# Optimization experiments

Hardware: AMD Instinct MI355X
Metric: run time of the kernel (lower is better)

The kernel has to match this reference:

```python
import jax, jax.numpy as jnp
import numpy as np

N = 8192
E = 262144
EMBD = 64
NIN = 16
K = 4

def setup_inputs() -> dict:
    key = jax.random.key(0)
    k1, k2, k3, k4 = jax.random.split(key, 4)
    node_features = jax.random.normal(k1, (N, EMBD), dtype=jnp.float32)
    edge_index = jax.random.randint(k2, (2, E), 0, N, dtype=jnp.int64)
    edge_weights = jax.random.uniform(k3, (E,), dtype=jnp.float32)
    # xavier_uniform for Emb [embdsize, nin]
    limit = float(np.sqrt(6.0 / (EMBD + NIN)))
    Emb = jax.random.uniform(k4, (EMBD, NIN), dtype=jnp.float32, minval=-limit, maxval=limit)
    return {"node_features": node_features, "edge_index": edge_index,
            "edge_weights": edge_weights, "Emb": Emb}

def reference(node_features, edge_index, edge_weights, Emb):
    # embed: [N, embdsize] @ [embdsize, nin] -> [N, nin]
    x = node_features @ Emb
    # matching torch fancy-index assignment)
    A = jnp.zeros((N, N), dtype=x.dtype).at[edge_index[0], edge_index[1]].set(edge_weights)
    def step(h, _):
        h = A @ h
        return h, h
    _, data_out = jax.lax.scan(step, x, None, length=K)  # [K, N, nin]
    return data_out
```

## Files before the change

kernel.cpp:

```cpp
#include <hip/hip_runtime.h>

#define N_NODES 8192
#define E_EDGES 262144
#define EMBDSZ  64
#define NIN     16
#define K_STEPS 4
#define ROWCAP  96
#define NBLK    1024
#define NTHR    256
#define NGRP    32
#define GRPSZ   32

typedef unsigned long long u64;
typedef unsigned u32;
typedef float f32x4 __attribute__((ext_vector_type(4)));

#define AT_LOAD(p)     __hip_atomic_load((p), __ATOMIC_RELAXED, __HIP_MEMORY_SCOPE_AGENT)
#define AT_STORE(p, v) __hip_atomic_store((p), (v), __ATOMIC_RELAXED, __HIP_MEMORY_SCOPE_AGENT)
#define AT_ADD(p, v)   __hip_atomic_fetch_add((p), (v), __ATOMIC_RELAXED, __HIP_MEMORY_SCOPE_AGENT)

__device__ __forceinline__ void store_f4_sc1(float* p, f32x4 v) {
    asm volatile("global_store_dwordx4 %0, %1, off sc1" :: "v"(p), "v"(v) : "memory");
}

__global__ void init_kernel(u32* __restrict__ cursor, u32* __restrict__ bar) {
    int t = threadIdx.x;
    uint4 z = make_uint4(0, 0, 0, 0);
    #pragma unroll
    for (int i = 0; i < 8; ++i) ((uint4*)cursor)[t + i * NTHR] = z;
    #pragma unroll
    for (int i = 0; i < 2; ++i) ((uint4*)bar)[t + i * NTHR] = z;
}

__global__ void embed_scatter_kernel(const float* __restrict__ nf,
                                     const float* __restrict__ emb,
                                     const int*   __restrict__ ei,
                                     const float* __restrict__ ew,
                                     float* __restrict__ x0,
                                     u32*   __restrict__ cursor,
                                     u64*   __restrict__ rowdat) {
    __shared__ float semb[EMBDSZ * NIN];
    const int b = blockIdx.x, tid = threadIdx.x;
    for (int i = tid; i < EMBDSZ * NIN; i += NTHR) semb[i] = emb[i];
    __syncthreads();
    int gt = b * NTHR + tid;
    {
        int o = gt >> 1, half = gt & 1;
        int n = o >> 4, jj = o & 15;
        const f32x4* nfp = (const f32x4*)(nf + n * EMBDSZ + half * 32);
        const float* ep  = semb + half * 32 * NIN + jj;
        float acc = 0.f;
        #pragma unroll
        for (int k8 = 0; k8 < 8; ++k8) {
            f32x4 a = nfp[k8];
            acc += a.x * ep[(k8 * 4 + 0) * NIN] + a.y * ep[(k8 * 4 + 1) * NIN]
                 + a.z * ep[(k8 * 4 + 2) * NIN] + a.w * ep[(k8 * 4 + 3) * NIN];
        }
        acc += __shfl_xor(acc, 1);
        if (half == 0) x0[o] = acc;
    }
    {
        int e = gt;
        u32 r  = (u32)ei[e];
        u32 c  = (u32)ei[E_EDGES + e];
        u32 wb = __float_as_uint(ew[e]);
        u32 slot = atomicAdd(&cursor[r], 1u);
        if (slot < ROWCAP)
            rowdat[(size_t)r * ROWCAP + slot] =
                ((u64)wb << 32) | (u64)(c << 18) | (u64)(u32)e;
    }
}

__device__ __forceinline__ void grid_barrier(u32* bar, u32 phase) {
    asm volatile("s_waitcnt vmcnt(0)" ::: "memory");
    __syncthreads();
    if (threadIdx.x == 0) {
        u32 g = (u32)blockIdx.x >> 5;
        if (AT_ADD(&bar[g * 16], 1u) == phase * GRPSZ - 1u) {
            if (AT_ADD(&bar[512], 1u) == phase * NGRP - 1u) {
                #pragma unroll
                for (u32 gg = 0; gg < NGRP; ++gg)
                    AT_STORE(&bar[528 + gg * 16], phase);
            }
        }
        while (AT_LOAD(&bar[528 + g * 16]) < phase) __builtin_amdgcn_s_sleep(1);
    }
    __syncthreads();
}

__global__ void __launch_bounds__(NTHR, 4) spmm_persist(
    const u32*   __restrict__ cursor,
    const u64*   __restrict__ rowdat,
    const float* __restrict__ x0,
    float* __restrict__ out,
    u32*   __restrict__ bar)
{
    __shared__ u64 srow[4][2][ROWCAP];
    const int b = blockIdx.x, tid = threadIdx.x;
    const int wid = tid >> 6, lane = tid & 63;
    const int slane = lane & 15, f4 = lane >> 4;
    const int wave = b * 4 + wid;

    u32 len[2];
    #pragma unroll
    for (int rr = 0; rr < 2; ++rr) {
        int row = wave * 2 + rr;
        u32 L = min(cursor[row], (u32)ROWCAP);
        len[rr] = L;
        const u64* rp = rowdat + (size_t)row * ROWCAP;
        for (u32 i = lane; i < L; i += 64) srow[wid][rr][i] = rp[i];
    }
    #pragma unroll
    for (int rr = 0; rr < 2; ++rr) {
        u32 L = len[rr];
        for (u32 i = lane; i < L; i += 64) {
            u64 v = srow[wid][rr][i];
            u32 lo = (u32)v;
            bool dead = false;
            for (u32 q = 0; q < L; ++q) {
                u32 o = (u32)srow[wid][rr][q];
                dead |= ((o >> 18) == (lo >> 18)) && (o > lo);
            }
            if (dead) srow[wid][rr][i] = (u64)lo;
        }
    }
    const float* hin = x0;
    for (int k = 0; k < K_STEPS; ++k) {
        if (k > 0) grid_barrier(bar, (u32)k);
        float* hout = out + (size_t)k * N_NODES * NIN;
        #pragma unroll
        for (int rr = 0; rr < 2; ++rr) {
            int row = wave * 2 + rr;
            u32 L = len[rr];
            f32x4 acc = {0.f, 0.f, 0.f, 0.f};
            for (u32 i = slane; i < L; i += 16) {
                u64 v = srow[wid][rr][i];
                float w = __uint_as_float((u32)(v >> 32));
                u32 c = ((u32)v) >> 18;
                f32x4 h = *(const f32x4*)&hin[c * NIN + f4 * 4];
                acc += w * h;
            }
            #pragma unroll
            for (int d = 1; d < 16; d <<= 1) {
                acc.x += __shfl_xor(acc.x, d);
                acc.y += __shfl_xor(acc.y, d);
                acc.z += __shfl_xor(acc.z, d);
                acc.w += __shfl_xor(acc.w, d);
            }
            if (slane == 0) store_f4_sc1(&hout[row * NIN + f4 * 4], acc);
        }
        hin = hout;
    }
}

extern "C" void kernel_launch(void* const* d_in, const int* in_sizes, int n_in,
                              void* d_out, int out_size, void* d_ws, size_t ws_size,
                              hipStream_t stream) {
    (void)in_sizes; (void)n_in; (void)out_size; (void)ws_size;
    const float* nf  = (const float*)d_in[0];
    const int*   ei  = (const int*)d_in[1];
    const float* ew  = (const float*)d_in[2];
    const float* emb = (const float*)d_in[3];
    float* out = (float*)d_out;

    char* ws = (char*)d_ws;
    size_t off = 0;
    auto alloc = [&](size_t bytes) {
        void* p = ws + off;
        off += (bytes + 255) & ~(size_t)255;
        return p;
    };
    u64*   rowdat = (u64*)alloc((size_t)N_NODES * ROWCAP * 8);
    float* x0     = (float*)alloc((size_t)N_NODES * NIN * 4);
    u32*   cursor = (u32*)alloc((size_t)N_NODES * 4);
    u32*   bar    = (u32*)alloc(8192);

    init_kernel<<<1, NTHR, 0, stream>>>(cursor, bar);
    embed_scatter_kernel<<<1024, NTHR, 0, stream>>>(nf, emb, ei, ew, x0, cursor, rowdat);
    spmm_persist<<<NBLK, NTHR, 0, stream>>>(cursor, rowdat, x0, out, bar);
}
```

Before: 58.08 us.

## Fuse embed/scatter into persistent kernel and replace grid barriers with per-row progress flags

Merges the embedding/scatter kernel and the persistent SpMM kernel into one launch, separated by a single flat atomic-counter grid barrier. The per-step hierarchical grid barriers are replaced by dataflow sync: each wave publishes a per-row progress counter after writing its rows, and before each step it polls the counters of the source rows in its adjacency list. This removes one kernel launch and lets waves proceed as soon as their neighbors are ready. In exchange it adds many polled atomic loads per step and a contended single counter for the first barrier.

Result: slower. 144.8 us (+149.3%).

```diff
diff --git a/kernel.cpp b/kernel.cpp
--- a/kernel.cpp
+++ b/kernel.cpp
@@ -8,8 +8,6 @@
 #define ROWCAP  96
 #define NBLK    1024
 #define NTHR    256
-#define NGRP    32
-#define GRPSZ   32
 
 typedef unsigned long long u64;
 typedef unsigned u32;
@@ -22,28 +20,44 @@
 __device__ __forceinline__ void store_f4_sc1(float* p, f32x4 v) {
     asm volatile("global_store_dwordx4 %0, %1, off sc1" :: "v"(p), "v"(v) : "memory");
 }
-
-__global__ void init_kernel(u32* __restrict__ cursor, u32* __restrict__ bar) {
-    int t = threadIdx.x;
-    uint4 z = make_uint4(0, 0, 0, 0);
-    #pragma unroll
-    for (int i = 0; i < 8; ++i) ((uint4*)cursor)[t + i * NTHR] = z;
-    #pragma unroll
-    for (int i = 0; i < 2; ++i) ((uint4*)bar)[t + i * NTHR] = z;
+__device__ __forceinline__ void store_u64_sc1(u64* p, u64 v) {
+    asm volatile("global_store_dwordx2 %0, %1, off sc1" :: "v"(p), "v"(v) : "memory");
+}
+__device__ __forceinline__ void store_f32_sc1(float* p, float v) {
+    asm volatile("global_store_dword %0, %1, off sc1" :: "v"(p), "v"(v) : "memory");
 }
 
-__global__ void embed_scatter_kernel(const float* __restrict__ nf,
-                                     const float* __restrict__ emb,
-                                     const int*   __restrict__ ei,
-                                     const float* __restrict__ ew,
-                                     float* __restrict__ x0,
-                                     u32*   __restrict__ cursor,
-                                     u64*   __restrict__ rowdat) {
+__global__ void init_kernel(u32* __restrict__ cursor, u32* __restrict__ prog,
+                            u32* __restrict__ done) {
+    int t = blockIdx.x * NTHR + threadIdx.x;
+    cursor[t] = 0;
+    prog[t]   = 0;
+    if (t == 0) *done = 0;
+}
+
+__global__ void __launch_bounds__(NTHR, 4) mega_kernel(
+    const float* __restrict__ nf,
+    const float* __restrict__ emb,
+    const int*   __restrict__ ei,
+    const float* __restrict__ ew,
+    float* __restrict__ out,
+    float* __restrict__ x0,
+    u32*   __restrict__ cursor,
+    u64*   __restrict__ rowdat,
+    u32*   __restrict__ prog,
+    u32*   __restrict__ done)
+{
     __shared__ float semb[EMBDSZ * NIN];
+    __shared__ u64   srow[4][2][ROWCAP];
+
     const int b = blockIdx.x, tid = threadIdx.x;
+    const int wid = tid >> 6, lane = tid & 63;
+    const int slane = lane & 15, f4 = lane >> 4;
+    const int wave = b * 4 + wid;
+    const int gt = b * NTHR + tid;
+
     for (int i = tid; i < EMBDSZ * NIN; i += NTHR) semb[i] = emb[i];
     __syncthreads();
-    int gt = b * NTHR + tid;
     {
         int o = gt >> 1, half = gt & 1;
         int n = o >> 4, jj = o & 15;
@@ -57,49 +71,24 @@
                  + a.z * ep[(k8 * 4 + 2) * NIN] + a.w * ep[(k8 * 4 + 3) * NIN];
         }
         acc += __shfl_xor(acc, 1);
-        if (half == 0) x0[o] = acc;
+        if (half == 0) store_f32_sc1(&x0[o], acc);
     }
     {
-        int e = gt;
-        u32 r  = (u32)ei[e];
-        u32 c  = (u32)ei[E_EDGES + e];
-        u32 wb = __float_as_uint(ew[e]);
+        u32 r  = (u32)ei[gt];
+        u32 c  = (u32)ei[E_EDGES + gt];
+        u32 wb = __float_as_uint(ew[gt]);
         u32 slot = atomicAdd(&cursor[r], 1u);
         if (slot < ROWCAP)
-            rowdat[(size_t)r * ROWCAP + slot] =
-                ((u64)wb << 32) | (u64)(c << 18) | (u64)(u32)e;
+            store_u64_sc1(&rowdat[(size_t)r * ROWCAP + slot],
+                          ((u64)wb << 32) | (u64)(c << 18) | (u64)(u32)gt);
     }
-}
-
-__device__ __forceinline__ void grid_barrier(u32* bar, u32 phase) {
     asm volatile("s_waitcnt vmcnt(0)" ::: "memory");
     __syncthreads();
-    if (threadIdx.x == 0) {
-        u32 g = (u32)blockIdx.x >> 5;
-        if (AT_ADD(&bar[g * 16], 1u) == phase * GRPSZ - 1u) {
-            if (AT_ADD(&bar[512], 1u) == phase * NGRP - 1u) {
-                #pragma unroll
-                for (u32 gg = 0; gg < NGRP; ++gg)
-                    AT_STORE(&bar[528 + gg * 16], phase);
-            }
-        }
-        while (AT_LOAD(&bar[528 + g * 16]) < phase) __builtin_amdgcn_s_sleep(1);
+    if (tid == 0) {
+        AT_ADD(done, 1u);
+        while (AT_LOAD(done) < (u32)NBLK) __builtin_amdgcn_s_sleep(2);
     }
     __syncthreads();
-}
-
-__global__ void __launch_bounds__(NTHR, 4) spmm_persist(
-    const u32*   __restrict__ cursor,
-    const u64*   __restrict__ rowdat,
-    const float* __restrict__ x0,
-    float* __restrict__ out,
-    u32*   __restrict__ bar)
-{
-    __shared__ u64 srow[4][2][ROWCAP];
-    const int b = blockIdx.x, tid = threadIdx.x;
-    const int wid = tid >> 6, lane = tid & 63;
-    const int slane = lane & 15, f4 = lane >> 4;
-    const int wave = b * 4 + wid;
 
     u32 len[2];
     #pragma unroll
@@ -109,10 +98,6 @@
         len[rr] = L;
         const u64* rp = rowdat + (size_t)row * ROWCAP;
         for (u32 i = lane; i < L; i += 64) srow[wid][rr][i] = rp[i];
-    }
-    #pragma unroll
-    for (int rr = 0; rr < 2; ++rr) {
-        u32 L = len[rr];
         for (u32 i = lane; i < L; i += 64) {
             u64 v = srow[wid][rr][i];
             u32 lo = (u32)v;
@@ -124,14 +109,25 @@
             if (dead) srow[wid][rr][i] = (u64)lo;
         }
     }
+
     const float* hin = x0;
     for (int k = 0; k < K_STEPS; ++k) {
-        if (k > 0) grid_barrier(bar, (u32)k);
         float* hout = out + (size_t)k * N_NODES * NIN;
         #pragma unroll
         for (int rr = 0; rr < 2; ++rr) {
             int row = wave * 2 + rr;
             u32 L = len[rr];
+            if (k > 0) {
+                for (;;) {
+                    bool ok = true;
+                    for (u32 i = lane; i < L; i += 64) {
+                        u32 src = ((u32)srow[wid][rr][i]) >> 18;
+                        ok &= (AT_LOAD(&prog[src]) >= (u32)k);
+                    }
+                    if (__all(ok)) break;
+                    __builtin_amdgcn_s_sleep(1);
+                }
+            }
             f32x4 acc = {0.f, 0.f, 0.f, 0.f};
             for (u32 i = slane; i < L; i += 16) {
                 u64 v = srow[wid][rr][i];
@@ -148,6 +144,11 @@
                 acc.w += __shfl_xor(acc.w, d);
             }
             if (slane == 0) store_f4_sc1(&hout[row * NIN + f4 * 4], acc);
+        }
+        asm volatile("s_waitcnt vmcnt(0)" ::: "memory");
+        if (lane == 0) {
+            AT_STORE(&prog[wave * 2],     (u32)(k + 1));
+            AT_STORE(&prog[wave * 2 + 1], (u32)(k + 1));
         }
         hin = hout;
     }
@@ -173,9 +174,10 @@
     u64*   rowdat = (u64*)alloc((size_t)N_NODES * ROWCAP * 8);
     float* x0     = (float*)alloc((size_t)N_NODES * NIN * 4);
     u32*   cursor = (u32*)alloc((size_t)N_NODES * 4);
-    u32*   bar    = (u32*)alloc(8192);
+    u32*   prog   = (u32*)alloc((size_t)N_NODES * 4);
+    u32*   done   = (u32*)alloc(256);
 
-    init_kernel<<<1, NTHR, 0, stream>>>(cursor, bar);
-    embed_scatter_kernel<<<1024, NTHR, 0, stream>>>(nf, emb, ei, ew, x0, cursor, rowdat);
-    spmm_persist<<<NBLK, NTHR, 0, stream>>>(cursor, rowdat, x0, out, bar);
+    init_kernel<<<32, NTHR, 0, stream>>>(cursor, prog, done);
+    mega_kernel<<<NBLK, NTHR, 0, stream>>>(nf, emb, ei, ew, out, x0,
+                                           cursor, rowdat, prog, done);
 }
```
